# Performance work log

Measured on AMD Instinct MI355X. Metric: run time of the kernel, lower is better.

## Reference

```python
import jax, jax.numpy as jnp
import numpy as np

B, S, D = 2, 2048, 1024
H, DH = 16, 64
EPS = 1e-5

def setup_inputs() -> dict:
    key = jax.random.key(0)
    ks = jax.random.split(key, 8)
    s = 0.02
    return {
        "x": jax.random.normal(ks[0], (B, S, D), dtype=jnp.float32),
        "ln_gamma": jnp.ones((D,), jnp.float32),
        "ln_beta": jnp.zeros((D,), jnp.float32),
        "wq": jax.random.normal(ks[1], (D, H * DH), jnp.float32) * s,
        "bq": jnp.zeros((H * DH,), jnp.float32),
        "wk": jax.random.normal(ks[2], (D, H * DH), jnp.float32) * s,
        "bk": jnp.zeros((H * DH,), jnp.float32),
        "wv": jax.random.normal(ks[3], (D, H * DH), jnp.float32) * s,
        "bv": jnp.zeros((H * DH,), jnp.float32),
        "wo": jax.random.normal(ks[4], (H * DH, D), jnp.float32) * s,
        "bo": jnp.zeros((D,), jnp.float32),
    }

def reference(x, ln_gamma, ln_beta, wq, bq, wk, bk, wv, bv, wo, bo):
    # Pre-LayerNorm over d_model
    mu = jnp.mean(x, axis=-1, keepdims=True)
    var = jnp.var(x, axis=-1, keepdims=True)
    xn = (x - mu) * jax.lax.rsqrt(var + EPS) * ln_gamma + ln_beta

    b, s, _ = xn.shape
    q = (xn @ wq + bq).reshape(b, s, H, DH)
    k = (xn @ wk + bk).reshape(b, s, H, DH)
    v = (xn @ wv + bv).reshape(b, s, H, DH)

    scale = jnp.sqrt(jnp.float32(DH))
    scores = jnp.einsum('bihd,bjhd->bhij', q, k) / scale  # [b,h,s,s]
    att = jax.nn.softmax(scores, axis=-1)
    out = jnp.einsum('bhij,bjhd->bihd', att, v).reshape(b, s, H * DH)
    return out @ wo + bo
```

## Files before the change

kernel.cpp:

```cpp
#include <hip/hip_runtime.h>
#include <math.h>

#define SEQ   2048
#define DM    1024
#define NHEAD 16
#define HD    64
#define NTOK  4096
#define EPS   1e-5f
#define SCALE_C 0.18033688f

typedef __attribute__((ext_vector_type(8))) short v8s;
typedef __attribute__((ext_vector_type(4))) short v4s;
typedef __attribute__((ext_vector_type(4))) float v4f;
typedef unsigned short ushort_t;

#define GLOAD16(g, l) __builtin_amdgcn_global_load_lds( \
    (const __attribute__((address_space(1))) unsigned int*)(g), \
    (__attribute__((address_space(3))) unsigned int*)(l), 16, 0, 0)

#if defined(__has_builtin)
#if __has_builtin(__builtin_amdgcn_mfma_f32_16x16x16_bf16)
#define MFMA16(va, vb, vc) __builtin_amdgcn_mfma_f32_16x16x16_bf16(va, vb, vc, 0, 0, 0)
#elif __has_builtin(__builtin_amdgcn_mfma_f32_16x16x16bf16_1k)
#define MFMA16(va, vb, vc) __builtin_amdgcn_mfma_f32_16x16x16bf16_1k(va, vb, vc, 0, 0, 0)
#endif
#endif
#ifndef MFMA16
__device__ __forceinline__ v4f mfma16_asm(v4s a, v4s b, v4f c) {
  asm volatile("s_nop 2\n\tv_mfma_f32_16x16x16_bf16 %0, %1, %2, %0\n\ts_nop 4"
               : "+v"(c) : "v"(a), "v"(b));
  return c;
}
#define MFMA16(va, vb, vc) mfma16_asm(va, vb, vc)
#endif

__device__ __forceinline__ unsigned short f2bf(float f) {
  union { float f; unsigned u; } v; v.f = f;
  unsigned r = v.u + 0x7FFFu + ((v.u >> 16) & 1u);
  return (unsigned short)(r >> 16);
}

__device__ __forceinline__ unsigned pack2_bf16(float a, float b) {
  union { float f; unsigned u; } ua, ub;
  ua.f = a; ub.f = b;
  return __builtin_amdgcn_perm(ub.u + 0x8000u, ua.u + 0x8000u, 0x07060302u);
}

__global__ __launch_bounds__(256) void prep_kernel(
    const float* __restrict__ x, const float* __restrict__ g,
    const float* __restrict__ be, ushort_t* __restrict__ y,
    const float* __restrict__ w0, const float* __restrict__ w1,
    const float* __restrict__ w2, const float* __restrict__ w3,
    ushort_t* __restrict__ o0, ushort_t* __restrict__ o1,
    ushort_t* __restrict__ o2, ushort_t* __restrict__ o3) {
  __shared__ float red[8];
  __shared__ float mu_s, rs_s;
  __shared__ float tile[64][65];
  const int t = threadIdx.x;
  if (blockIdx.x < NTOK) {
    const int row = blockIdx.x;
    const float4 v = ((const float4*)(x + (size_t)row * DM))[t];
    float s  = v.x + v.y + v.z + v.w;
    float ss = v.x*v.x + v.y*v.y + v.z*v.z + v.w*v.w;
    #pragma unroll
    for (int off = 32; off > 0; off >>= 1) {
      s  += __shfl_down(s,  off, 64);
      ss += __shfl_down(ss, off, 64);
    }
    const int wid = t >> 6, lane = t & 63;
    if (lane == 0) { red[wid] = s; red[4 + wid] = ss; }
    __syncthreads();
    if (t == 0) {
      const float S  = red[0] + red[1] + red[2] + red[3];
      const float SS = red[4] + red[5] + red[6] + red[7];
      const float mu  = S * (1.0f / DM);
      const float var = SS * (1.0f / DM) - mu * mu;
      mu_s = mu; rs_s = rsqrtf(var + EPS);
    }
    __syncthreads();
    const float mu = mu_s, r = rs_s;
    const float4 gv = ((const float4*)g)[t];
    const float4 bv = ((const float4*)be)[t];
    ushort4 o;
    o.x = f2bf((v.x - mu) * r * gv.x + bv.x);
    o.y = f2bf((v.y - mu) * r * gv.y + bv.y);
    o.z = f2bf((v.z - mu) * r * gv.z + bv.z);
    o.w = f2bf((v.w - mu) * r * gv.w + bv.w);
    *(ushort4*)(y + (size_t)row * DM + t * 4) = o;
  } else {
    const int i = blockIdx.x - NTOK;
    const int z = i >> 8;
    const float* w = (z==0) ? w0 : (z==1) ? w1 : (z==2) ? w2 : w3;
    ushort_t* o    = (z==0) ? o0 : (z==1) ? o1 : (z==2) ? o2 : o3;
    const int n0 = (i & 15) * 64, k0 = ((i >> 4) & 15) * 64;
    const int r = t >> 4, c4 = (t & 15) * 4;
    #pragma unroll
    for (int ii = 0; ii < 4; ++ii) {
      const float4 v = *(const float4*)(w + (size_t)(k0 + r + ii*16) * DM + n0 + c4);
      tile[r + ii*16][c4 + 0] = v.x;
      tile[r + ii*16][c4 + 1] = v.y;
      tile[r + ii*16][c4 + 2] = v.z;
      tile[r + ii*16][c4 + 3] = v.w;
    }
    __syncthreads();
    #pragma unroll
    for (int ii = 0; ii < 4; ++ii) {
      const int n = r + ii*16;
      ushort4 o4;
      o4.x = f2bf(tile[c4 + 0][n]);
      o4.y = f2bf(tile[c4 + 1][n]);
      o4.z = f2bf(tile[c4 + 2][n]);
      o4.w = f2bf(tile[c4 + 3][n]);
      *(ushort4*)(o + (size_t)(n0 + n) * DM + k0 + c4) = o4;
    }
  }
}

__device__ __forceinline__ void gemm_main(ushort_t* lsa, ushort_t* lsb,
    const ushort_t* A, const ushort_t* WT, int m0, int n0, v4f acc[4][4]) {
  const int tid = threadIdx.x;
  const int wid = tid >> 6, lane = tid & 63;
  const int mh = (wid & 1) << 6, nh = (wid >> 1) << 6;
  const int r16 = lane & 15, quad = lane >> 4;
  const int srow = lane >> 2, sch = lane & 3;
  for (int k0 = 0; k0 < DM; k0 += 32) {
    __syncthreads();
    #pragma unroll
    for (int j = 0; j < 2; ++j) {
      const int o = wid * 2 + j;
      GLOAD16(A  + (size_t)(m0 + o*16 + srow) * DM + k0 + sch*8, lsa + o*512);
      GLOAD16(WT + (size_t)(n0 + o*16 + srow) * DM + k0 + sch*8, lsb + o*512);
    }
    __syncthreads();
    v8s af[4], bfr[4];
    #pragma unroll
    for (int i = 0; i < 4; ++i) {
      af[i]  = *(const v8s*)(lsa + (mh + i*16 + r16)*32 + quad*8);
      bfr[i] = *(const v8s*)(lsb + (nh + i*16 + r16)*32 + quad*8);
    }
    #pragma unroll
    for (int i = 0; i < 4; ++i)
      #pragma unroll
      for (int j = 0; j < 4; ++j)
        acc[i][j] = __builtin_amdgcn_mfma_f32_16x16x32_bf16(af[i], bfr[j], acc[i][j], 0, 0, 0);
  }
}

__global__ __launch_bounds__(256, 2) void gemm_qkv(const ushort_t* __restrict__ xn,
    const ushort_t* __restrict__ wtq, const ushort_t* __restrict__ wtk, const ushort_t* __restrict__ wtv,
    const float* __restrict__ bq, const float* __restrict__ bk, const float* __restrict__ bv,
    ushort_t* __restrict__ qo, ushort_t* __restrict__ ko, ushort_t* __restrict__ vto) {
  __shared__ ushort_t lsa[128*32];
  __shared__ ushort_t lsb[128*32];
  const int z = blockIdx.z;
  const ushort_t* WT = (z == 0) ? wtq : (z == 1) ? wtk : wtv;
  const float* bias  = (z == 0) ? bq  : (z == 1) ? bk  : bv;
  const int m0 = blockIdx.y * 128, n0 = blockIdx.x * 128;
  v4f acc[4][4];
  #pragma unroll
  for (int i = 0; i < 4; ++i)
    #pragma unroll
    for (int j = 0; j < 4; ++j) acc[i][j] = (v4f){0.f, 0.f, 0.f, 0.f};
  gemm_main(lsa, lsb, xn, WT, m0, n0, acc);
  const int tid = threadIdx.x, wid = tid >> 6, lane = tid & 63;
  const int mh = (wid & 1) << 6, nh = (wid >> 1) << 6;
  const int r16 = lane & 15, quad = lane >> 4;
  if (z < 2) {
    ushort_t* out = (z == 0) ? qo : ko;
    const float sc = (z == 0) ? SCALE_C : 1.0f;
    #pragma unroll
    for (int bn = 0; bn < 4; ++bn) {
      const int col = n0 + nh + bn*16 + r16;
      const float bb = bias[col];
      #pragma unroll
      for (int am = 0; am < 4; ++am) {
        const int tb = m0 + mh + am*16 + quad*4;
        #pragma unroll
        for (int r = 0; r < 4; ++r)
          out[(size_t)(tb + r) * DM + col] = f2bf((acc[am][bn][r] + bb) * sc);
      }
    }
  } else {
    #pragma unroll
    for (int bn = 0; bn < 4; ++bn) {
      const int col = n0 + nh + bn*16 + r16;
      const float bb = bias[col];
      const int h = col >> 6, d = col & 63;
      #pragma unroll
      for (int am = 0; am < 4; ++am) {
        const int tb = m0 + mh + am*16 + quad*4;
        const int b = tb >> 11, t = tb & 2047;
        const int bh = b * NHEAD + h;
        ushort4 o4;
        o4.x = f2bf(acc[am][bn][0] + bb);
        o4.y = f2bf(acc[am][bn][1] + bb);
        o4.z = f2bf(acc[am][bn][2] + bb);
        o4.w = f2bf(acc[am][bn][3] + bb);
        const size_t idx = (size_t)bh * 131072 + (size_t)(t >> 6) * 4096 +
                           (size_t)((((t >> 4) & 3) * 4) + (d >> 4)) * 256 +
                           ((t >> 2) & 3) * 64 + (d & 15) * 4;
        *(ushort4*)(vto + idx) = o4;
      }
    }
  }
}

__global__ __launch_bounds__(256, 2) void gemm_out(const ushort_t* __restrict__ A,
    const ushort_t* __restrict__ WT, const float* __restrict__ bias,
    float* __restrict__ out) {
  __shared__ ushort_t lsa[128*32];
  __shared__ ushort_t lsb[128*32];
  const int m0 = blockIdx.y * 128, n0 = blockIdx.x * 128;
  v4f acc[4][4];
  #pragma unroll
  for (int i = 0; i < 4; ++i)
    #pragma unroll
    for (int j = 0; j < 4; ++j) acc[i][j] = (v4f){0.f, 0.f, 0.f, 0.f};
  gemm_main(lsa, lsb, A, WT, m0, n0, acc);
  const int tid = threadIdx.x, wid = tid >> 6, lane = tid & 63;
  const int mh = (wid & 1) << 6, nh = (wid >> 1) << 6;
  const int r16 = lane & 15, quad = lane >> 4;
  #pragma unroll
  for (int bn = 0; bn < 4; ++bn) {
    const int col = n0 + nh + bn*16 + r16;
    const float bb = bias[col];
    #pragma unroll
    for (int am = 0; am < 4; ++am) {
      const int tb = m0 + mh + am*16 + quad*4;
      #pragma unroll
      for (int r = 0; r < 4; ++r)
        out[(size_t)(tb + r) * DM + col] = acc[am][bn][r] + bb;
    }
  }
}

#define OHALF ((size_t)32 * 2048 * 64)
#define LHALF (32 * 2048)
template<int SPLIT>
__global__ __launch_bounds__(256, 8) void attn_kernel(
    const ushort_t* __restrict__ Q, const ushort_t* __restrict__ K,
    const ushort_t* __restrict__ Vt, ushort_t* __restrict__ O,
    float* __restrict__ Opart, float* __restrict__ lpart) {
  __shared__ ushort_t kbuf[2][8*512];
  __shared__ ushort_t vbuf[2][16*256];
  const int tid = threadIdx.x, wid = tid >> 6, lane = tid & 63;
  const int r16 = lane & 15, quad = lane >> 4;
  const int q0 = blockIdx.x * 64, bh = blockIdx.y;
  const int half = SPLIT ? blockIdx.z : 0;
  const int b = bh >> 4, h = bh & 15;
  const ushort_t* gQ = Q + (size_t)b * SEQ * DM + h * HD;
  const ushort_t* gK = K + (size_t)b * SEQ * DM + h * HD;
  const ushort_t* gV = Vt + (size_t)bh * 131072;

  const int qtok = q0 + wid * 16 + r16;
  const v8s qf0 = *(const v8s*)(gQ + (size_t)qtok * DM + quad * 8);
  const v8s qf1 = *(const v8s*)(gQ + (size_t)qtok * DM + 32 + quad * 8);
  v4f acco[4];
  #pragma unroll
  for (int i = 0; i < 4; ++i) acco[i] = (v4f){0.f, 0.f, 0.f, 0.f};
  float lrun = 0.f;

  const int NIT = SPLIT ? (SEQ / 128) : (SEQ / 64);
  const int kt0 = half * NIT;

  auto stage = [&](int bs, int kt) {
    const int k0 = kt * 64;
    #pragma unroll
    for (int j = 0; j < 2; ++j) {
      const int o = wid * 2 + j;
      GLOAD16(gK + (size_t)(k0 + (o >> 1) * 16 + r16) * DM + (o & 1) * 32 + quad * 8,
              kbuf[bs] + o * 512);
    }
    #pragma unroll
    for (int j = 0; j < 2; ++j) {
      const int o = wid * 2 + j;
      GLOAD16(gV + (size_t)kt * 4096 + o * 512 + lane * 8, vbuf[bs] + o * 512);
    }
  };

  stage(0, kt0);
  __syncthreads();

  for (int it = 0; it < NIT; ++it) {
    const int cur = it & 1;
    stage(cur ^ 1, kt0 + ((it + 1 == NIT) ? 0 : it + 1));

    v4f sacc[4];
    #pragma unroll
    for (int g = 0; g < 4; ++g) sacc[g] = (v4f){0.f, 0.f, 0.f, 0.f};
    #pragma unroll
    for (int g = 0; g < 4; ++g) {
      const v8s ka0 = *(const v8s*)(kbuf[cur] + (g*2 + 0) * 512 + lane * 8);
      const v8s ka1 = *(const v8s*)(kbuf[cur] + (g*2 + 1) * 512 + lane * 8);
      sacc[g] = __builtin_amdgcn_mfma_f32_16x16x32_bf16(ka0, qf0, sacc[g], 0, 0, 0);
      sacc[g] = __builtin_amdgcn_mfma_f32_16x16x32_bf16(ka1, qf1, sacc[g], 0, 0, 0);
    }

    float ls = 0.f;
    v4s pfrag[4];
    #pragma unroll
    for (int g = 0; g < 4; ++g) {
      float e0 = __builtin_amdgcn_exp2f(sacc[g][0]);
      float e1 = __builtin_amdgcn_exp2f(sacc[g][1]);
      float e2 = __builtin_amdgcn_exp2f(sacc[g][2]);
      float e3 = __builtin_amdgcn_exp2f(sacc[g][3]);
      ls += (e0 + e1) + (e2 + e3);
      union { v4s s; uint2 u; } pk;
      pk.u.x = pack2_bf16(e0, e1);
      pk.u.y = pack2_bf16(e2, e3);
      pfrag[g] = pk.s;
    }
    ls += __shfl_xor(ls, 16, 64);
    ls += __shfl_xor(ls, 32, 64);
    lrun += ls;

    #pragma unroll
    for (int dg = 0; dg < 4; ++dg) {
      #pragma unroll
      for (int g = 0; g < 4; ++g) {
        const v4s vf = *(const v4s*)(vbuf[cur] + (g*4 + dg) * 256 + quad * 64 + r16 * 4);
        acco[dg] = MFMA16(vf, pfrag[g], acco[dg]);
      }
    }

    __syncthreads();
  }

  if (SPLIT) {
    float* Op = Opart + half * OHALF + ((size_t)bh * SEQ + qtok) * 64;
    #pragma unroll
    for (int dg = 0; dg < 4; ++dg)
      *(v4f*)(Op + dg*16 + quad*4) = acco[dg];
    if (quad == 0) lpart[half * LHALF + bh * SEQ + qtok] = lrun;
  } else {
    const float inv = 1.f / lrun;
    ushort_t* gO = O + (size_t)b * SEQ * DM + h * HD;
    #pragma unroll
    for (int dg = 0; dg < 4; ++dg) {
      ushort4 o4;
      o4.x = f2bf(acco[dg][0] * inv);
      o4.y = f2bf(acco[dg][1] * inv);
      o4.z = f2bf(acco[dg][2] * inv);
      o4.w = f2bf(acco[dg][3] * inv);
      *(ushort4*)(gO + (size_t)qtok * DM + dg*16 + quad*4) = o4;
    }
  }
}

__global__ __launch_bounds__(256) void combine_kernel(
    const float* __restrict__ Opart, const float* __restrict__ lpart,
    ushort_t* __restrict__ ob) {
  const int tok = blockIdx.x;
  const int b = tok >> 11, t = tok & 2047;
  const int dm0 = threadIdx.x * 4;
  const int h = dm0 >> 6, d = dm0 & 63;
  const int bh = b * NHEAD + h;
  const size_t idx = ((size_t)bh * SEQ + t) * 64 + d;
  const float4 a = *(const float4*)(Opart + idx);
  const float4 c = *(const float4*)(Opart + OHALF + idx);
  const float l = lpart[bh * SEQ + t] + lpart[LHALF + bh * SEQ + t];
  const float inv = 1.f / l;
  ushort4 o4;
  o4.x = f2bf((a.x + c.x) * inv);
  o4.y = f2bf((a.y + c.y) * inv);
  o4.z = f2bf((a.z + c.z) * inv);
  o4.w = f2bf((a.w + c.w) * inv);
  *(ushort4*)(ob + (size_t)tok * DM + dm0) = o4;
}

extern "C" void kernel_launch(void* const* d_in, const int* in_sizes, int n_in,
                              void* d_out, int out_size, void* d_ws, size_t ws_size,
                              hipStream_t stream) {
  const float* x     = (const float*)d_in[0];
  const float* gamma = (const float*)d_in[1];
  const float* beta  = (const float*)d_in[2];
  const float* wq    = (const float*)d_in[3];
  const float* bq    = (const float*)d_in[4];
  const float* wk    = (const float*)d_in[5];
  const float* bk    = (const float*)d_in[6];
  const float* wv    = (const float*)d_in[7];
  const float* bv    = (const float*)d_in[8];
  const float* wo    = (const float*)d_in[9];
  const float* bo    = (const float*)d_in[10];
  float* out = (float*)d_out;

  unsigned char* w8 = (unsigned char*)d_ws;
  const size_t MB = 1024 * 1024;
  ushort_t* xn  = (ushort_t*)(w8 + 0 * MB);
  ushort_t* qb  = (ushort_t*)(w8 + 8 * MB);
  ushort_t* kb  = (ushort_t*)(w8 + 16 * MB);
  ushort_t* vt  = (ushort_t*)(w8 + 24 * MB);
  ushort_t* wtq = (ushort_t*)(w8 + 32 * MB);
  ushort_t* wtk = (ushort_t*)(w8 + 34 * MB);
  ushort_t* wtv = (ushort_t*)(w8 + 36 * MB);
  ushort_t* wto = (ushort_t*)(w8 + 38 * MB);
  float* Opart  = (float*)(w8 + 40 * MB);
  float* lpart  = (float*)(w8 + 72 * MB);
  ushort_t* ob  = xn;

  prep_kernel<<<dim3(NTOK + 1024), dim3(256), 0, stream>>>(
      x, gamma, beta, xn, wq, wk, wv, wo, wtq, wtk, wtv, wto);
  gemm_qkv<<<dim3(8, 32, 3), dim3(256), 0, stream>>>(xn, wtq, wtk, wtv, bq, bk, bv, qb, kb, vt);
  if (ws_size >= 73 * MB) {
    attn_kernel<1><<<dim3(SEQ / 64, 2 * NHEAD, 2), dim3(256), 0, stream>>>(
        qb, kb, vt, nullptr, Opart, lpart);
    combine_kernel<<<dim3(NTOK), dim3(256), 0, stream>>>(Opart, lpart, ob);
  } else {
    attn_kernel<0><<<dim3(SEQ / 64, 2 * NHEAD, 1), dim3(256), 0, stream>>>(
        qb, kb, vt, ob, nullptr, nullptr);
  }
  gemm_out<<<dim3(8, 32, 1), dim3(256), 0, stream>>>(ob, wto, bo, out);
}
```

Before: 218.5 us.

## Replace double-buffered LDS DMA with register-staged single-buffer prefetch in attention

Attention K/V tiles are now staged through a single LDS buffer. The next tile is prefetched into registers with ordinary global loads during compute, then written to LDS between two barriers. This halves LDS usage per block, which may raise occupancy, and drops the direct global-to-LDS loads. In exchange it uses extra VGPRs for the staged data, adds a second barrier per iteration, and exposes the LDS write latency.

```diff
diff --git a/kernel.cpp b/kernel.cpp
--- a/kernel.cpp
+++ b/kernel.cpp
@@ -241,8 +241,8 @@
     const ushort_t* __restrict__ Q, const ushort_t* __restrict__ K,
     const ushort_t* __restrict__ Vt, ushort_t* __restrict__ O,
     float* __restrict__ Opart, float* __restrict__ lpart) {
-  __shared__ ushort_t kbuf[2][8*512];
-  __shared__ ushort_t vbuf[2][16*256];
+  __shared__ ushort_t kbuf[8*512];
+  __shared__ ushort_t vbuf[8*512];
   const int tid = threadIdx.x, wid = tid >> 6, lane = tid & 63;
   const int r16 = lane & 15, quad = lane >> 4;
   const int q0 = blockIdx.x * 64, bh = blockIdx.y;
@@ -262,36 +262,39 @@
 
   const int NIT = SPLIT ? (SEQ / 128) : (SEQ / 64);
   const int kt0 = half * NIT;
-
-  auto stage = [&](int bs, int kt) {
-    const int k0 = kt * 64;
-    #pragma unroll
-    for (int j = 0; j < 2; ++j) {
-      const int o = wid * 2 + j;
-      GLOAD16(gK + (size_t)(k0 + (o >> 1) * 16 + r16) * DM + (o & 1) * 32 + quad * 8,
-              kbuf[bs] + o * 512);
-    }
-    #pragma unroll
-    for (int j = 0; j < 2; ++j) {
-      const int o = wid * 2 + j;
-      GLOAD16(gV + (size_t)kt * 4096 + o * 512 + lane * 8, vbuf[bs] + o * 512);
-    }
-  };
-
-  stage(0, kt0);
+  const int o0 = wid * 2, o1 = wid * 2 + 1;
+  const ushort_t* srcK0 = gK + (size_t)((o0 >> 1) * 16 + r16) * DM + (o0 & 1) * 32 + quad * 8;
+  const ushort_t* srcK1 = gK + (size_t)((o1 >> 1) * 16 + r16) * DM + (o1 & 1) * 32 + quad * 8;
+  const ushort_t* srcV  = gV + lane * 8;
+
+  {
+    const int k0 = kt0 * 64;
+    GLOAD16(srcK0 + (size_t)k0 * DM, kbuf + o0 * 512);
+    GLOAD16(srcK1 + (size_t)k0 * DM, kbuf + o1 * 512);
+    GLOAD16(srcV + (size_t)kt0 * 4096 + o0 * 512, vbuf + o0 * 512);
+    GLOAD16(srcV + (size_t)kt0 * 4096 + o1 * 512, vbuf + o1 * 512);
+  }
   __syncthreads();
 
   for (int it = 0; it < NIT; ++it) {
-    const int cur = it & 1;
-    stage(cur ^ 1, kt0 + ((it + 1 == NIT) ? 0 : it + 1));
+    const int kt = kt0 + it;
+    uint4 rk0, rk1, rv0, rv1;
+    const bool pf = (it + 1 < NIT);
+    if (pf) {
+      const size_t k0n = (size_t)(kt + 1) * 64;
+      rk0 = *(const uint4*)(srcK0 + k0n * DM);
+      rk1 = *(const uint4*)(srcK1 + k0n * DM);
+      rv0 = *(const uint4*)(srcV + (size_t)(kt + 1) * 4096 + o0 * 512);
+      rv1 = *(const uint4*)(srcV + (size_t)(kt + 1) * 4096 + o1 * 512);
+    }
 
     v4f sacc[4];
     #pragma unroll
     for (int g = 0; g < 4; ++g) sacc[g] = (v4f){0.f, 0.f, 0.f, 0.f};
     #pragma unroll
     for (int g = 0; g < 4; ++g) {
-      const v8s ka0 = *(const v8s*)(kbuf[cur] + (g*2 + 0) * 512 + lane * 8);
-      const v8s ka1 = *(const v8s*)(kbuf[cur] + (g*2 + 1) * 512 + lane * 8);
+      const v8s ka0 = *(const v8s*)(kbuf + (g*2 + 0) * 512 + lane * 8);
+      const v8s ka1 = *(const v8s*)(kbuf + (g*2 + 1) * 512 + lane * 8);
       sacc[g] = __builtin_amdgcn_mfma_f32_16x16x32_bf16(ka0, qf0, sacc[g], 0, 0, 0);
       sacc[g] = __builtin_amdgcn_mfma_f32_16x16x32_bf16(ka1, qf1, sacc[g], 0, 0, 0);
     }
@@ -318,11 +321,18 @@
     for (int dg = 0; dg < 4; ++dg) {
       #pragma unroll
       for (int g = 0; g < 4; ++g) {
-        const v4s vf = *(const v4s*)(vbuf[cur] + (g*4 + dg) * 256 + quad * 64 + r16 * 4);
+        const v4s vf = *(const v4s*)(vbuf + (g*4 + dg) * 256 + quad * 64 + r16 * 4);
         acco[dg] = MFMA16(vf, pfrag[g], acco[dg]);
       }
     }
 
+    __syncthreads();
+    if (pf) {
+      *(uint4*)(kbuf + o0 * 512 + lane * 8) = rk0;
+      *(uint4*)(kbuf + o1 * 512 + lane * 8) = rk1;
+      *(uint4*)(vbuf + o0 * 512 + lane * 8) = rv0;
+      *(uint4*)(vbuf + o1 * 512 + lane * 8) = rv1;
+    }
     __syncthreads();
   }
 
```

New measurement: 215.5 us. About the same (-1.4%).
